# Optimization experiments

Hardware: AMD Instinct MI355X
Metric: run time of the kernel (lower is better)

The kernel has to match this reference:

```python
import jax, jax.numpy as jnp
import numpy as np

B, T, C = 2, 2048, 2048
N_HEAD, N_KV = 32, 8
HD = C // N_HEAD  # 64
N_REP = N_HEAD // N_KV  # 4
ROPE_BASE = 10000.0


def setup_inputs() -> dict:
    key = jax.random.key(0)
    ks = jax.random.split(key, 5)
    s = 0.02
    return {
        "x": jax.random.normal(ks[0], (B, T, C), jnp.float32),
        "Wq": jax.random.normal(ks[1], (C, N_HEAD * HD), jnp.float32) * s,
        "Wk": jax.random.normal(ks[2], (C, N_KV * HD), jnp.float32) * s,
        "Wv": jax.random.normal(ks[3], (C, N_KV * HD), jnp.float32) * s,
        "Wo": jax.random.normal(ks[4], (N_HEAD * HD, C), jnp.float32) * s,
    }


def _rope_cos_sin(seq_len, head_dim, dtype):
    inv_freq = 1.0 / (ROPE_BASE ** (jnp.arange(0, head_dim, 2, dtype=jnp.float32) / head_dim))
    t = jnp.arange(seq_len, dtype=jnp.float32)
    freqs = t[:, None] * inv_freq[None, :]           # (T, hd/2)
    emb = jnp.concatenate([freqs, freqs], axis=-1)    # (T, hd)
    return jnp.cos(emb).astype(dtype), jnp.sin(emb).astype(dtype)


def _rotate_half(x):
    h = x.shape[-1] // 2
    return jnp.concatenate([-x[..., h:], x[..., :h]], axis=-1)


def reference(x, Wq, Wk, Wv, Wo):
    b, t, c = x.shape
    # projections -> (B, H, T, hd)
    q = (x @ Wq).reshape(b, t, N_HEAD, HD).transpose(0, 2, 1, 3)
    k = (x @ Wk).reshape(b, t, N_KV, HD).transpose(0, 2, 1, 3)
    v = (x @ Wv).reshape(b, t, N_KV, HD).transpose(0, 2, 1, 3)

    cos, sin = _rope_cos_sin(t, HD, x.dtype)          # (T, hd)
    q = q * cos + _rotate_half(q) * sin
    k = k * cos + _rotate_half(k) * sin

    # GQA: group query heads (B, n_kv, n_rep, T, hd) against shared KV (no repeat materialization)
    qg = q.reshape(b, N_KV, N_REP, t, HD)
    scale = 1.0 / jnp.sqrt(jnp.asarray(HD, x.dtype))
    scores = jnp.einsum('bgrqd,bgkd->bgrqk', qg, k) * scale  # (B, n_kv, n_rep, T, T)
    causal = jnp.tril(jnp.ones((t, t), bool))
    scores = jnp.where(causal, scores, jnp.asarray(-jnp.inf, scores.dtype))
    probs = jax.nn.softmax(scores, axis=-1)
    out = jnp.einsum('bgrqk,bgkd->bgrqd', probs, v)          # (B, n_kv, n_rep, T, hd)
    out = out.reshape(b, N_HEAD, t, HD).transpose(0, 2, 1, 3).reshape(b, t, N_HEAD * HD)
    return out @ Wo
```

## Files before the change

kernel.cpp:

```cpp
#include <hip/hip_runtime.h>
#include <stdint.h>

#define Bn 2
#define Tn 2048
#define Cn 2048
#define NHEAD 32
#define NKVH 8
#define HDIM 64
#define Mn (Bn*Tn)
#define NQKV 3072
#define KOFF 2048
#define VOFF 2560

typedef __attribute__((ext_vector_type(8))) short bf16x8;
typedef __attribute__((ext_vector_type(4))) float f32x4;

#define AS1 __attribute__((address_space(1)))
#define AS3 __attribute__((address_space(3)))
#define GLOAD_LDS16(g, l) __builtin_amdgcn_global_load_lds((const AS1 void*)(g), (AS3 void*)(l), 16, 0, 0)

#define SCL 0.18033688f

__device__ __forceinline__ unsigned short f2bf(float f) {
    union { float f; unsigned u; } v; v.f = f;
    return (unsigned short)((v.u + 0x7fffu + ((v.u >> 16) & 1u)) >> 16);
}
__device__ __forceinline__ float bf2f(unsigned short b) {
    union { unsigned u; float f; } v; v.u = ((unsigned)b) << 16;
    return v.f;
}

__global__ void convert_f32_bf16(const float* __restrict__ src,
                                 unsigned short* __restrict__ dst, int n4) {
    int i = blockIdx.x * blockDim.x + threadIdx.x;
    if (i >= n4) return;
    float4 f = ((const float4*)src)[i];
    ushort4 o;
    o.x = f2bf(f.x); o.y = f2bf(f.y); o.z = f2bf(f.z); o.w = f2bf(f.w);
    ((ushort4*)dst)[i] = o;
}

__global__ void transpose_convert(const float* __restrict__ src,
                                  unsigned short* __restrict__ dst, int K, int N) {
    __shared__ float tile[32][33];
    int k0 = blockIdx.x * 32, n0 = blockIdx.y * 32;
    int tx = threadIdx.x, ty = threadIdx.y;
    #pragma unroll
    for (int yy = 0; yy < 32; yy += 8)
        tile[ty + yy][tx] = src[(size_t)(k0 + ty + yy) * N + n0 + tx];
    __syncthreads();
    #pragma unroll
    for (int yy = 0; yy < 32; yy += 8)
        dst[(size_t)(n0 + ty + yy) * K + k0 + tx] = f2bf(tile[tx][ty + yy]);
}

__global__ void rope_tables(float* __restrict__ ct, float* __restrict__ st) {
    int i = blockIdx.x * blockDim.x + threadIdx.x;
    int t = i >> 5, d = i & 31;
    float invf = powf(10000.0f, -(float)d / 32.0f);
    float f = (float)t * invf;
    ct[i] = cosf(f);
    st[i] = sinf(f);
}

__global__ void rope_apply(unsigned short* __restrict__ qkv,
                           const float* __restrict__ ct, const float* __restrict__ st) {
    int i = blockIdx.x * blockDim.x + threadIdx.x;
    int p = i & 31;
    int h = (i >> 5) % 40;
    int bt = i / (40 * 32);
    int t = bt & (Tn - 1);
    size_t base = (size_t)bt * NQKV + h * 64;
    float v0 = bf2f(qkv[base + p]);
    float v1 = bf2f(qkv[base + p + 32]);
    float c = ct[t * 32 + p], s = st[t * 32 + p];
    float scl = (h < 32) ? SCL : 1.0f;
    qkv[base + p]      = f2bf((v0 * c - v1 * s) * scl);
    qkv[base + p + 32] = f2bf((v1 * c + v0 * s) * scl);
}

__global__ void transpose_v(const unsigned short* __restrict__ qkv,
                            unsigned short* __restrict__ vt) {
    __shared__ unsigned short tile[32][33];
    int t0 = blockIdx.x * 32;
    int b = blockIdx.y >> 3, kvh = blockIdx.y & 7;
    int d0 = blockIdx.z * 32;
    int tx = threadIdx.x, ty = threadIdx.y;
    #pragma unroll
    for (int yy = 0; yy < 32; yy += 8)
        tile[ty + yy][tx] = qkv[(size_t)(b * Tn + t0 + ty + yy) * NQKV + VOFF + kvh * 64 + d0 + tx];
    __syncthreads();
    #pragma unroll
    for (int yy = 0; yy < 32; yy += 8)
        vt[(size_t)((b * 8 + kvh) * 64 + d0 + ty + yy) * Tn + t0 + tx] = tile[tx][ty + yy];
}

template <bool BF16OUT>
__global__ __launch_bounds__(256) void gemm_bt(
    const unsigned short* __restrict__ A, const unsigned short* __restrict__ Bt,
    unsigned short* __restrict__ outb, float* __restrict__ outf, int M, int N, int K) {
    __shared__ unsigned short sA[128 * 32];
    __shared__ unsigned short sB[128 * 32];
    int tid = threadIdx.x;
    int wid = tid >> 6, lane = tid & 63;
    int wr = wid >> 1, wc = wid & 1;
    int g = lane >> 4, r16 = lane & 15;
    int brow = blockIdx.y * 128, bcol = blockIdx.x * 128;

    f32x4 acc[4][4];
    #pragma unroll
    for (int m = 0; m < 4; m++)
        #pragma unroll
        for (int n = 0; n < 4; n++) acc[m][n] = (f32x4){0.f, 0.f, 0.f, 0.f};

    for (int k0 = 0; k0 < K; k0 += 32) {
        __syncthreads();
        #pragma unroll
        for (int j = 0; j < 2; j++) {
            int cs = wid * 2 + j;
            int bo = cs * 1024 + lane * 16;
            int row = bo >> 6;
            int ce = (bo & 63) >> 1;
            const unsigned short* ga = A + (size_t)(brow + row) * K + k0 + ce;
            const unsigned short* gb = Bt + (size_t)(bcol + row) * K + k0 + ce;
            GLOAD_LDS16(ga, (char*)sA + cs * 1024);
            GLOAD_LDS16(gb, (char*)sB + cs * 1024);
        }
        __syncthreads();
        bf16x8 av[4], bv[4];
        #pragma unroll
        for (int m = 0; m < 4; m++)
            av[m] = *(const bf16x8*)&sA[(wr * 64 + m * 16 + r16) * 32 + g * 8];
        #pragma unroll
        for (int n = 0; n < 4; n++)
            bv[n] = *(const bf16x8*)&sB[(wc * 64 + n * 16 + r16) * 32 + g * 8];
        #pragma unroll
        for (int m = 0; m < 4; m++)
            #pragma unroll
            for (int n = 0; n < 4; n++)
                acc[m][n] = __builtin_amdgcn_mfma_f32_16x16x32_bf16(av[m], bv[n], acc[m][n], 0, 0, 0);
    }

    #pragma unroll
    for (int m = 0; m < 4; m++) {
        #pragma unroll
        for (int n = 0; n < 4; n++) {
            int row0 = brow + wr * 64 + m * 16 + g * 4;
            int col = bcol + wc * 64 + n * 16 + r16;
            #pragma unroll
            for (int r = 0; r < 4; r++) {
                float v = acc[m][n][r];
                if (BF16OUT)
                    outb[(size_t)(row0 + r) * N + col] = f2bf(v);
                else
                    outf[(size_t)(row0 + r) * N + col] = v;
            }
        }
    }
}

__device__ __forceinline__ void flash_step(
    const bf16x8 (&qf)[2], float (&pl)[4], f32x4 (&oo)[4],
    const unsigned short* __restrict__ sK, const unsigned short* __restrict__ sVt,
    unsigned short* __restrict__ sPw, int g, int r16, int wid, bool masked) {
    f32x4 s[4];
    #pragma unroll
    for (int n = 0; n < 4; n++) {
        s[n] = (f32x4){0.f, 0.f, 0.f, 0.f};
        #pragma unroll
        for (int kc = 0; kc < 2; kc++) {
            int kv = n * 16 + r16;
            int bo = (kv * 128 + kc * 64 + g * 16) ^ ((kv & 7) << 4);
            bf16x8 kf = *(const bf16x8*)((const char*)sK + bo);
            s[n] = __builtin_amdgcn_mfma_f32_16x16x32_bf16(qf[kc], kf, s[n], 0, 0, 0);
        }
    }
    if (masked) {
        #pragma unroll
        for (int n = 0; n < 4; n++)
            #pragma unroll
            for (int r = 0; r < 4; r++)
                s[n][r] = (n * 16 + r16 <= wid * 16 + g * 4 + r) ? s[n][r] : -1e30f;
    }
    #pragma unroll
    for (int n = 0; n < 4; n++)
        #pragma unroll
        for (int r = 0; r < 4; r++) s[n][r] = exp2f(s[n][r]);
    #pragma unroll
    for (int r = 0; r < 4; r++)
        pl[r] += (s[0][r] + s[1][r]) + (s[2][r] + s[3][r]);
    #pragma unroll
    for (int n = 0; n < 4; n++)
        #pragma unroll
        for (int r = 0; r < 4; r++) {
            int prow = g * 4 + r;
            int bo = (prow * 128 + (n * 16 + r16) * 2) ^ ((prow & 7) << 4);
            union { float f; unsigned u; } pv; pv.f = s[n][r];
            *(unsigned short*)((char*)sPw + bo) = (unsigned short)(pv.u >> 16);
        }
    #pragma unroll
    for (int dt = 0; dt < 4; dt++) {
        #pragma unroll
        for (int kc = 0; kc < 2; kc++) {
            int bo = (r16 * 128 + kc * 64 + g * 16) ^ ((r16 & 7) << 4);
            bf16x8 pf = *(const bf16x8*)((const char*)sPw + bo);
            int dd = dt * 16 + r16;
            int bo2 = (dd * 128 + kc * 64 + g * 16) ^ ((dd & 7) << 4);
            bf16x8 vf = *(const bf16x8*)((const char*)sVt + bo2);
            oo[dt] = __builtin_amdgcn_mfma_f32_16x16x32_bf16(pf, vf, oo[dt], 0, 0, 0);
        }
    }
}

__global__ __launch_bounds__(256, 4) void attn_fwd(
    const unsigned short* __restrict__ qkv, const unsigned short* __restrict__ vt,
    unsigned short* __restrict__ att) {
    __shared__ unsigned short sK[2][64 * 64];
    __shared__ unsigned short sVt[2][64 * 64];
    __shared__ unsigned short sP[4][16 * 64];

    int tid = threadIdx.x;
    int wid = tid >> 6, lane = tid & 63;
    int g = lane >> 4, r16 = lane & 15;
    int qp = blockIdx.x;
    int bh = blockIdx.y;
    int b = bh >> 5, qh = bh & 31, kvh = qh >> 2;
    int qtA = qp, qtB = 31 - qp;

    const unsigned short* base = qkv + (size_t)b * Tn * NQKV;
    const unsigned short* kg = base + KOFF + kvh * 64;
    const unsigned short* vg = vt + (size_t)((b * 8 + kvh) * 64) * Tn;

    int cs = 0, stg_coff = 0, stg_row = 0;
    {
    }

    bf16x8 qfA[2], qfB[2];
    {
        int qrA = qtA * 64 + wid * 16 + r16;
        int qrB = qtB * 64 + wid * 16 + r16;
        #pragma unroll
        for (int kc = 0; kc < 2; kc++) {
            qfA[kc] = *(const bf16x8*)(base + (size_t)qrA * NQKV + qh * 64 + kc * 32 + g * 8);
            qfB[kc] = *(const bf16x8*)(base + (size_t)qrB * NQKV + qh * 64 + kc * 32 + g * 8);
        }
    }

    float plA[4], plB[4];
    f32x4 oA[4], oB[4];
    #pragma unroll
    for (int r = 0; r < 4; r++) { plA[r] = 0.f; plB[r] = 0.f; }
    #pragma unroll
    for (int d = 0; d < 4; d++) {
        oA[d] = (f32x4){0.f, 0.f, 0.f, 0.f};
        oB[d] = (f32x4){0.f, 0.f, 0.f, 0.f};
    }

    unsigned short* sPw = &sP[wid][0];

    #pragma unroll
    for (int jj = 0; jj < 2; jj++) {
        int c = wid * 2 + jj;
        int bo = c * 1024 + lane * 16;
        int row = bo >> 7;
        int coff = (bo & 127) ^ ((row & 7) << 4);
        GLOAD_LDS16(kg + (size_t)row * NQKV + (coff >> 1), (char*)&sK[0][0] + c * 1024);
        GLOAD_LDS16(vg + (size_t)row * Tn + (coff >> 1), (char*)&sVt[0][0] + c * 1024);
    }
    __syncthreads();

    int cur = 0;
    for (int j = 0; j <= qtB; j++) {
        if (j < qtB) {
            int nxt = cur ^ 1;
            #pragma unroll
            for (int jj = 0; jj < 2; jj++) {
                int c = wid * 2 + jj;
                int bo = c * 1024 + lane * 16;
                int row = bo >> 7;
                int coff = (bo & 127) ^ ((row & 7) << 4);
                GLOAD_LDS16(kg + (size_t)((j + 1) * 64 + row) * NQKV + (coff >> 1),
                            (char*)&sK[nxt][0] + c * 1024);
                GLOAD_LDS16(vg + (size_t)row * Tn + (j + 1) * 64 + (coff >> 1),
                            (char*)&sVt[nxt][0] + c * 1024);
            }
        }
        const unsigned short* sKc = &sK[cur][0];
        const unsigned short* sVc = &sVt[cur][0];
        if (j <= qtA) flash_step(qfA, plA, oA, sKc, sVc, sPw, g, r16, wid, j == qtA);
        flash_step(qfB, plB, oB, sKc, sVc, sPw, g, r16, wid, j == qtB);
        __syncthreads();
        cur ^= 1;
    }

    float lA[4], lB[4];
    #pragma unroll
    for (int r = 0; r < 4; r++) {
        float vA = plA[r], vB = plB[r];
        #pragma unroll
        for (int msk = 1; msk < 16; msk <<= 1) {
            vA += __shfl_xor(vA, msk, 64);
            vB += __shfl_xor(vB, msk, 64);
        }
        lA[r] = 1.0f / vA;
        lB[r] = 1.0f / vB;
    }
    #pragma unroll
    for (int dt = 0; dt < 4; dt++)
        #pragma unroll
        for (int r = 0; r < 4; r++) {
            int qgA = qtA * 64 + wid * 16 + g * 4 + r;
            int qgB = qtB * 64 + wid * 16 + g * 4 + r;
            att[(size_t)(b * Tn + qgA) * Cn + qh * 64 + dt * 16 + r16] = f2bf(oA[dt][r] * lA[r]);
            att[(size_t)(b * Tn + qgB) * Cn + qh * 64 + dt * 16 + r16] = f2bf(oB[dt][r] * lB[r]);
        }
}

extern "C" void kernel_launch(void* const* d_in, const int* in_sizes, int n_in,
                              void* d_out, int out_size, void* d_ws, size_t ws_size,
                              hipStream_t stream) {
    const float* x  = (const float*)d_in[0];
    const float* Wq = (const float*)d_in[1];
    const float* Wk = (const float*)d_in[2];
    const float* Wv = (const float*)d_in[3];
    const float* Wo = (const float*)d_in[4];
    float* out = (float*)d_out;

    char* w = (char*)d_ws;
    unsigned short* Xb    = (unsigned short*)w; w += (size_t)Mn * Cn * 2;
    unsigned short* Wqkvt = (unsigned short*)w; w += (size_t)NQKV * Cn * 2;
    unsigned short* Wot   = (unsigned short*)w; w += (size_t)Cn * Cn * 2;
    unsigned short* QKV   = (unsigned short*)w; w += (size_t)Mn * NQKV * 2;
    unsigned short* ATT   = (unsigned short*)w; w += (size_t)Mn * Cn * 2;
    unsigned short* Vt    = (unsigned short*)w; w += (size_t)Bn * NKVH * HDIM * Tn * 2;
    float* ct = (float*)w; w += (size_t)Tn * 32 * 4;
    float* st = (float*)w; w += (size_t)Tn * 32 * 4;

    convert_f32_bf16<<<(Mn * Cn / 4) / 256, 256, 0, stream>>>(x, Xb, Mn * Cn / 4);
    dim3 tb(32, 8);
    transpose_convert<<<dim3(64, 64), tb, 0, stream>>>(Wq, Wqkvt, Cn, 2048);
    transpose_convert<<<dim3(64, 16), tb, 0, stream>>>(Wk, Wqkvt + (size_t)2048 * Cn, Cn, 512);
    transpose_convert<<<dim3(64, 16), tb, 0, stream>>>(Wv, Wqkvt + (size_t)2560 * Cn, Cn, 512);
    transpose_convert<<<dim3(64, 64), tb, 0, stream>>>(Wo, Wot, Cn, 2048);
    rope_tables<<<(Tn * 32) / 256, 256, 0, stream>>>(ct, st);

    gemm_bt<true><<<dim3(NQKV / 128, Mn / 128), 256, 0, stream>>>(Xb, Wqkvt, QKV, nullptr, Mn, NQKV, Cn);
    rope_apply<<<(Mn * 40 * 32) / 256, 256, 0, stream>>>(QKV, ct, st);
    transpose_v<<<dim3(Tn / 32, Bn * NKVH, 2), tb, 0, stream>>>(QKV, Vt);
    attn_fwd<<<dim3(16, Bn * NHEAD), 256, 0, stream>>>(QKV, Vt, ATT);
    gemm_bt<false><<<dim3(Cn / 128, Mn / 128), 256, 0, stream>>>(ATT, Wot, nullptr, out, Mn, Cn, Cn);
}
```

Baseline: 246.8 us.

## Fuse RoPE into QKV GEMM epilogue, merge weight transposes, add MFMA priority

Applies the rotary embedding and the query scaling inside the QKV projection GEMM epilogue. Each warp's column tile of 64 holds both rotation halves, so the separate rope_apply pass that re-read and re-wrote Q and K is removed. The three Wq/Wk/Wv transpose launches become one kernel, which cuts launch overhead. s_setprio is raised around the attention MFMA blocks to favour matrix issue. The fused epilogue adds extra table loads and scattered bf16 stores inside the GEMM.

New measurement: 241.7 us. 2.1% less time.

```diff
diff --git a/kernel.cpp b/kernel.cpp
--- a/kernel.cpp
+++ b/kernel.cpp
@@ -54,6 +54,24 @@
         dst[(size_t)(n0 + ty + yy) * K + k0 + tx] = f2bf(tile[tx][ty + yy]);
 }
 
+__global__ void transpose_wqkv(const float* __restrict__ Wq, const float* __restrict__ Wk,
+                               const float* __restrict__ Wv, unsigned short* __restrict__ dst) {
+    __shared__ float tile[32][33];
+    int k0 = blockIdx.x * 32, n0 = blockIdx.y * 32;
+    const float* src; int srcN, c0;
+    if (n0 < 2048)      { src = Wq; srcN = 2048; c0 = n0; }
+    else if (n0 < 2560) { src = Wk; srcN = 512;  c0 = n0 - 2048; }
+    else                { src = Wv; srcN = 512;  c0 = n0 - 2560; }
+    int tx = threadIdx.x, ty = threadIdx.y;
+    #pragma unroll
+    for (int yy = 0; yy < 32; yy += 8)
+        tile[ty + yy][tx] = src[(size_t)(k0 + ty + yy) * srcN + c0 + tx];
+    __syncthreads();
+    #pragma unroll
+    for (int yy = 0; yy < 32; yy += 8)
+        dst[(size_t)(n0 + ty + yy) * Cn + k0 + tx] = f2bf(tile[tx][ty + yy]);
+}
+
 __global__ void rope_tables(float* __restrict__ ct, float* __restrict__ st) {
     int i = blockIdx.x * blockDim.x + threadIdx.x;
     int t = i >> 5, d = i & 31;
@@ -63,22 +81,6 @@
     st[i] = sinf(f);
 }
 
-__global__ void rope_apply(unsigned short* __restrict__ qkv,
-                           const float* __restrict__ ct, const float* __restrict__ st) {
-    int i = blockIdx.x * blockDim.x + threadIdx.x;
-    int p = i & 31;
-    int h = (i >> 5) % 40;
-    int bt = i / (40 * 32);
-    int t = bt & (Tn - 1);
-    size_t base = (size_t)bt * NQKV + h * 64;
-    float v0 = bf2f(qkv[base + p]);
-    float v1 = bf2f(qkv[base + p + 32]);
-    float c = ct[t * 32 + p], s = st[t * 32 + p];
-    float scl = (h < 32) ? SCL : 1.0f;
-    qkv[base + p]      = f2bf((v0 * c - v1 * s) * scl);
-    qkv[base + p + 32] = f2bf((v1 * c + v0 * s) * scl);
-}
-
 __global__ void transpose_v(const unsigned short* __restrict__ qkv,
                             unsigned short* __restrict__ vt) {
     __shared__ unsigned short tile[32][33];
@@ -95,10 +97,11 @@
         vt[(size_t)((b * 8 + kvh) * 64 + d0 + ty + yy) * Tn + t0 + tx] = tile[tx][ty + yy];
 }
 
-template <bool BF16OUT>
+template <bool BF16OUT, bool ROPE>
 __global__ __launch_bounds__(256) void gemm_bt(
     const unsigned short* __restrict__ A, const unsigned short* __restrict__ Bt,
-    unsigned short* __restrict__ outb, float* __restrict__ outf, int M, int N, int K) {
+    unsigned short* __restrict__ outb, float* __restrict__ outf, int M, int N, int K,
+    const float* __restrict__ ct, const float* __restrict__ st) {
     __shared__ unsigned short sA[128 * 32];
     __shared__ unsigned short sB[128 * 32];
     int tid = threadIdx.x;
@@ -141,19 +144,47 @@
                 acc[m][n] = __builtin_amdgcn_mfma_f32_16x16x32_bf16(av[m], bv[n], acc[m][n], 0, 0, 0);
     }
 
-    #pragma unroll
-    for (int m = 0; m < 4; m++) {
-        #pragma unroll
-        for (int n = 0; n < 4; n++) {
-            int row0 = brow + wr * 64 + m * 16 + g * 4;
-            int col = bcol + wc * 64 + n * 16 + r16;
-            #pragma unroll
-            for (int r = 0; r < 4; r++) {
-                float v = acc[m][n][r];
-                if (BF16OUT)
-                    outb[(size_t)(row0 + r) * N + col] = f2bf(v);
-                else
-                    outf[(size_t)(row0 + r) * N + col] = v;
+    if (ROPE) {
+        #pragma unroll
+        for (int m = 0; m < 4; m++) {
+            #pragma unroll
+            for (int n = 0; n < 2; n++) {
+                int col = bcol + wc * 64 + n * 16 + r16;
+                int p = col & 63;
+                bool isV = (col >= VOFF);
+                float scl = (col < KOFF) ? SCL : 1.0f;
+                #pragma unroll
+                for (int r = 0; r < 4; r++) {
+                    int row = brow + wr * 64 + m * 16 + g * 4 + r;
+                    int t = row & (Tn - 1);
+                    float v0 = acc[m][n][r], v1 = acc[m][n + 2][r];
+                    float o0, o1;
+                    if (isV) { o0 = v0; o1 = v1; }
+                    else {
+                        float c = ct[t * 32 + p], s = st[t * 32 + p];
+                        o0 = (v0 * c - v1 * s) * scl;
+                        o1 = (v1 * c + v0 * s) * scl;
+                    }
+                    outb[(size_t)row * N + col]      = f2bf(o0);
+                    outb[(size_t)row * N + col + 32] = f2bf(o1);
+                }
+            }
+        }
+    } else {
+        #pragma unroll
+        for (int m = 0; m < 4; m++) {
+            #pragma unroll
+            for (int n = 0; n < 4; n++) {
+                int row0 = brow + wr * 64 + m * 16 + g * 4;
+                int col = bcol + wc * 64 + n * 16 + r16;
+                #pragma unroll
+                for (int r = 0; r < 4; r++) {
+                    float v = acc[m][n][r];
+                    if (BF16OUT)
+                        outb[(size_t)(row0 + r) * N + col] = f2bf(v);
+                    else
+                        outf[(size_t)(row0 + r) * N + col] = v;
+                }
             }
         }
     }
@@ -164,6 +195,7 @@
     const unsigned short* __restrict__ sK, const unsigned short* __restrict__ sVt,
     unsigned short* __restrict__ sPw, int g, int r16, int wid, bool masked) {
     f32x4 s[4];
+    __builtin_amdgcn_s_setprio(1);
     #pragma unroll
     for (int n = 0; n < 4; n++) {
         s[n] = (f32x4){0.f, 0.f, 0.f, 0.f};
@@ -175,6 +207,7 @@
             s[n] = __builtin_amdgcn_mfma_f32_16x16x32_bf16(qf[kc], kf, s[n], 0, 0, 0);
         }
     }
+    __builtin_amdgcn_s_setprio(0);
     if (masked) {
         #pragma unroll
         for (int n = 0; n < 4; n++)
@@ -198,6 +231,7 @@
             union { float f; unsigned u; } pv; pv.f = s[n][r];
             *(unsigned short*)((char*)sPw + bo) = (unsigned short)(pv.u >> 16);
         }
+    __builtin_amdgcn_s_setprio(1);
     #pragma unroll
     for (int dt = 0; dt < 4; dt++) {
         #pragma unroll
@@ -210,6 +244,7 @@
             oo[dt] = __builtin_amdgcn_mfma_f32_16x16x32_bf16(pf, vf, oo[dt], 0, 0, 0);
         }
     }
+    __builtin_amdgcn_s_setprio(0);
 }
 
 __global__ __launch_bounds__(256, 4) void attn_fwd(
@@ -230,10 +265,6 @@
     const unsigned short* base = qkv + (size_t)b * Tn * NQKV;
     const unsigned short* kg = base + KOFF + kvh * 64;
     const unsigned short* vg = vt + (size_t)((b * 8 + kvh) * 64) * Tn;
-
-    int cs = 0, stg_coff = 0, stg_row = 0;
-    {
-    }
 
     bf16x8 qfA[2], qfB[2];
     {
@@ -338,15 +369,14 @@
 
     convert_f32_bf16<<<(Mn * Cn / 4) / 256, 256, 0, stream>>>(x, Xb, Mn * Cn / 4);
     dim3 tb(32, 8);
-    transpose_convert<<<dim3(64, 64), tb, 0, stream>>>(Wq, Wqkvt, Cn, 2048);
-    transpose_convert<<<dim3(64, 16), tb, 0, stream>>>(Wk, Wqkvt + (size_t)2048 * Cn, Cn, 512);
-    transpose_convert<<<dim3(64, 16), tb, 0, stream>>>(Wv, Wqkvt + (size_t)2560 * Cn, Cn, 512);
+    transpose_wqkv<<<dim3(64, 96), tb, 0, stream>>>(Wq, Wk, Wv, Wqkvt);
     transpose_convert<<<dim3(64, 64), tb, 0, stream>>>(Wo, Wot, Cn, 2048);
     rope_tables<<<(Tn * 32) / 256, 256, 0, stream>>>(ct, st);
 
-    gemm_bt<true><<<dim3(NQKV / 128, Mn / 128), 256, 0, stream>>>(Xb, Wqkvt, QKV, nullptr, Mn, NQKV, Cn);
-    rope_apply<<<(Mn * 40 * 32) / 256, 256, 0, stream>>>(QKV, ct, st);
+    gemm_bt<true, true><<<dim3(NQKV / 128, Mn / 128), 256, 0, stream>>>(
+        Xb, Wqkvt, QKV, nullptr, Mn, NQKV, Cn, ct, st);
     transpose_v<<<dim3(Tn / 32, Bn * NKVH, 2), tb, 0, stream>>>(QKV, Vt);
     attn_fwd<<<dim3(16, Bn * NHEAD), 256, 0, stream>>>(QKV, Vt, ATT);
-    gemm_bt<false><<<dim3(Cn / 128, Mn / 128), 256, 0, stream>>>(ATT, Wot, nullptr, out, Mn, Cn, Cn);
-}
+    gemm_bt<false, false><<<dim3(Cn / 128, Mn / 128), 256, 0, stream>>>(
+        ATT, Wot, nullptr, out, Mn, Cn, Cn, nullptr, nullptr);
+}
```
